# Optimization experiments

Hardware: AMD Instinct MI355X
Metric: run time of the kernel (lower is better)

The kernel has to match this reference:

```python
import jax, jax.numpy as jnp
import numpy as np

D_MODEL = 1024
NUM_HEADS = 16
D_HEAD = D_MODEL // NUM_HEADS
BATCH = 4
SEQ = 2048
NEG_INF = -1e30


def setup_inputs() -> dict:
    key = jax.random.key(0)
    k_x, k_q, k_k, k_v, k_o = jax.random.split(key, 5)
    scale = 1.0 / np.sqrt(D_MODEL)
    x = jax.random.normal(k_x, (BATCH, SEQ, D_MODEL), dtype=jnp.float32)
    Qw = jax.random.normal(k_q, (D_MODEL, D_MODEL), dtype=jnp.float32) * scale
    Kw = jax.random.normal(k_k, (D_MODEL, D_MODEL), dtype=jnp.float32) * scale
    Vw = jax.random.normal(k_v, (D_MODEL, D_MODEL), dtype=jnp.float32) * scale
    Ow = jax.random.normal(k_o, (D_MODEL, D_MODEL), dtype=jnp.float32) * scale
    padding_mask = jnp.zeros((BATCH, SEQ), dtype=bool)  # True = masked position
    return {"x": x, "Qw": Qw, "Kw": Kw, "Vw": Vw, "Ow": Ow, "padding_mask": padding_mask}


def reference(x, Qw, Kw, Vw, Ow, padding_mask):
    B, S, D = x.shape
    H, dh = NUM_HEADS, D_HEAD
    # torch Linear (no bias): y = x @ W.T
    q = jnp.einsum("bsd,ed->bse", x, Qw).reshape(B, S, H, dh)
    k = jnp.einsum("bsd,ed->bse", x, Kw).reshape(B, S, H, dh)
    v = jnp.einsum("bsd,ed->bse", x, Vw).reshape(B, S, H, dh)
    # scores: [B, H, Sq, Sk]
    score = jnp.einsum("bqhd,bkhd->bhqk", q, k) / jnp.sqrt(jnp.float32(dh))
    # causal mask (masked=True)
    causal = jnp.tril(jnp.ones((S, S), dtype=bool))  # True = keep
    score = jnp.where(causal[None, None, :, :], score, NEG_INF)
    # padding mask: True = masked key position
    score = jnp.where(padding_mask[:, None, None, :], NEG_INF, score)
    attn = jax.nn.softmax(score, axis=-1)  # dropout=0.0 (eval mode)
    ctx = jnp.einsum("bhqk,bkhd->bqhd", attn, v).reshape(B, S, D)
    out = jnp.einsum("bsd,ed->bse", ctx, Ow)
    return out
```

## Files before the change

### kernel.cpp

```cpp
#include <hip/hip_runtime.h>
#include <hip/hip_bf16.h>

typedef __attribute__((ext_vector_type(8))) short short8;
typedef __attribute__((ext_vector_type(4))) float f32x4;

#define MFMA_BF16_16x16x32(a,b,c) __builtin_amdgcn_mfma_f32_16x16x32_bf16((a),(b),(c),0,0,0)

constexpr int B_  = 4;
constexpr int S_  = 2048;
constexpr int H_  = 16;
constexpr int DH_ = 64;
constexpr int D_  = 1024;
constexpr int M_  = B_ * S_;

__device__ __forceinline__ unsigned short f2bf(float f) {
  union { float f; unsigned u; } v; v.f = f;
  unsigned u = v.u;
  u += 0x7fffu + ((u >> 16) & 1u);
  return (unsigned short)(u >> 16);
}

__device__ __forceinline__ short8 cvt8(f32x4 a, f32x4 b) {
  union { __hip_bfloat162 h[4]; short8 s; } u;
  u.h[0] = __float22bfloat162_rn(make_float2(a[0], a[1]));
  u.h[1] = __float22bfloat162_rn(make_float2(a[2], a[3]));
  u.h[2] = __float22bfloat162_rn(make_float2(b[0], b[1]));
  u.h[3] = __float22bfloat162_rn(make_float2(b[2], b[3]));
  return u.s;
}

__device__ __forceinline__ unsigned pk2(float a, float b) {
  union { __hip_bfloat162 h; unsigned u; } z;
  z.h = __float22bfloat162_rn(make_float2(a, b));
  return z.u;
}

__global__ __launch_bounds__(256)
void cvt_pre(const float* __restrict__ x, unsigned short* __restrict__ xb,
             const float* __restrict__ Kw, const float* __restrict__ Vw,
             unsigned short* __restrict__ Kwb, unsigned short* __restrict__ Vwb) {
  const int bb = blockIdx.x;
  const float* s;
  unsigned short* d;
  size_t i;
  if (bb < 4096)      { s = x;  d = xb;  i = ((size_t)bb * 256 + threadIdx.x) * 8; }
  else if (bb < 4608) { s = Kw; d = Kwb; i = ((size_t)(bb - 4096) * 256 + threadIdx.x) * 8; }
  else                { s = Vw; d = Vwb; i = ((size_t)(bb - 4608) * 256 + threadIdx.x) * 8; }
  *(short8*)(d + i) = cvt8(*(const f32x4*)(s + i), *(const f32x4*)(s + i + 4));
}

__global__ __launch_bounds__(256)
void cvt_w(const float* __restrict__ s0, unsigned short* __restrict__ d0) {
  const size_t i = ((size_t)blockIdx.x * 256 + threadIdx.x) * 8;
  *(short8*)(d0 + i) = cvt8(*(const f32x4*)(s0 + i), *(const f32x4*)(s0 + i + 4));
}

__device__ __forceinline__ void stage16(const unsigned short* __restrict__ g,
                                        short* lds_wave_base, int lane) {
#if __has_builtin(__builtin_amdgcn_global_load_lds)
  __builtin_amdgcn_global_load_lds(
      (const __attribute__((address_space(1))) unsigned int*)g,
      (__attribute__((address_space(3))) unsigned int*)lds_wave_base, 16, 0, 0);
#else
  *(short8*)(lds_wave_base + lane * 8) = *(const short8*)g;
#endif
}

__global__ __launch_bounds__(256)
void gemm_bb(const unsigned short* __restrict__ xb,
             const unsigned short* __restrict__ Qwb,
             const unsigned short* __restrict__ Kwb,
             const unsigned short* __restrict__ Vwb,
             unsigned short* __restrict__ Qo, unsigned short* __restrict__ Ko,
             unsigned short* __restrict__ VTo, int haveQ) {
  __shared__ __align__(16) short As[128 * 32];
  __shared__ __align__(16) short Bs[128 * 32];

  const int nb  = blockIdx.x;
  const int sel = haveQ ? (nb >> 3) : 1 + (nb >> 3);
  const int n0  = (nb & 7) * 128;
  const unsigned short* Wb = (sel == 0) ? Qwb : (sel == 1) ? Kwb : Vwb;
  unsigned short* out      = (sel == 0) ? Qo  : (sel == 1) ? Ko  : VTo;
  const float scale = (sel == 0) ? 0.125f : 1.0f;
  const int epi = (sel == 2) ? 2 : 1;

  const int tid  = threadIdx.x;
  const int lane = tid & 63;
  const int w    = tid >> 6;
  const int quad = lane >> 4;
  const int l16  = lane & 15;
  const int wm   = (w >> 1) * 64;
  const int wn   = (w & 1) * 64;
  const int m0   = blockIdx.y * 128;

  const int srow = tid >> 2;
  const int scol = (tid & 3) * 8;

  f32x4 acc[4][4];
  #pragma unroll
  for (int i = 0; i < 4; ++i)
    #pragma unroll
    for (int j = 0; j < 4; ++j)
      acc[i][j] = (f32x4){0.f, 0.f, 0.f, 0.f};

  for (int k0 = 0; k0 < D_; k0 += 32) {
    __syncthreads();
    #pragma unroll
    for (int j = 0; j < 2; ++j) {
      const int row = j * 64 + srow;
      stage16(xb + (size_t)(m0 + row) * D_ + k0 + scol, As + j * 2048 + w * 512, lane);
      stage16(Wb + (size_t)(n0 + row) * D_ + k0 + scol, Bs + j * 2048 + w * 512, lane);
    }
    __syncthreads();

    short8 af[4], bf[4];
    #pragma unroll
    for (int i = 0; i < 4; ++i)
      af[i] = *(const short8*)(&As[(wm + i * 16 + l16) * 32 + quad * 8]);
    #pragma unroll
    for (int j = 0; j < 4; ++j)
      bf[j] = *(const short8*)(&Bs[(wn + j * 16 + l16) * 32 + quad * 8]);
    #pragma unroll
    for (int i = 0; i < 4; ++i)
      #pragma unroll
      for (int j = 0; j < 4; ++j)
        acc[i][j] = MFMA_BF16_16x16x32(af[i], bf[j], acc[i][j]);
  }

  #pragma unroll
  for (int i = 0; i < 4; ++i)
    #pragma unroll
    for (int j = 0; j < 4; ++j)
      #pragma unroll
      for (int r = 0; r < 4; ++r) {
        int m = m0 + wm + i * 16 + quad * 4 + r;
        int n = n0 + wn + j * 16 + l16;
        unsigned short bv = f2bf(acc[i][j][r] * scale);
        int b = m >> 11, s = m & (S_ - 1);
        int h = n >> 6,  d = n & (DH_ - 1);
        if (epi == 1)
          out[((size_t)(b * H_ + h) * S_ + s) * DH_ + d] = bv;
        else
          out[((size_t)(b * H_ + h) * DH_ + d) * S_ + s] = bv;
      }
}

__global__ __launch_bounds__(256)
void gemm_out_bb(const unsigned short* __restrict__ A,
                 const unsigned short* __restrict__ Wb,
                 float* __restrict__ out) {
  __shared__ __align__(16) short As[128 * 32];
  __shared__ __align__(16) short Bs[128 * 32];

  const int tid  = threadIdx.x;
  const int lane = tid & 63;
  const int w    = tid >> 6;
  const int quad = lane >> 4;
  const int l16  = lane & 15;
  const int wm   = (w >> 1) * 64;
  const int wn   = (w & 1) * 64;
  const int m0   = blockIdx.y * 128;
  const int n0   = blockIdx.x * 128;

  const int srow = tid >> 2;
  const int scol = (tid & 3) * 8;

  f32x4 acc[4][4];
  #pragma unroll
  for (int i = 0; i < 4; ++i)
    #pragma unroll
    for (int j = 0; j < 4; ++j)
      acc[i][j] = (f32x4){0.f, 0.f, 0.f, 0.f};

  for (int k0 = 0; k0 < D_; k0 += 32) {
    __syncthreads();
    #pragma unroll
    for (int j = 0; j < 2; ++j) {
      const int row = j * 64 + srow;
      stage16(A  + (size_t)(m0 + row) * D_ + k0 + scol, As + j * 2048 + w * 512, lane);
      stage16(Wb + (size_t)(n0 + row) * D_ + k0 + scol, Bs + j * 2048 + w * 512, lane);
    }
    __syncthreads();

    short8 af[4], bf[4];
    #pragma unroll
    for (int i = 0; i < 4; ++i)
      af[i] = *(const short8*)(&As[(wm + i * 16 + l16) * 32 + quad * 8]);
    #pragma unroll
    for (int j = 0; j < 4; ++j)
      bf[j] = *(const short8*)(&Bs[(wn + j * 16 + l16) * 32 + quad * 8]);
    #pragma unroll
    for (int i = 0; i < 4; ++i)
      #pragma unroll
      for (int j = 0; j < 4; ++j)
        acc[i][j] = MFMA_BF16_16x16x32(af[i], bf[j], acc[i][j]);
  }

  #pragma unroll
  for (int i = 0; i < 4; ++i)
    #pragma unroll
    for (int j = 0; j < 4; ++j)
      #pragma unroll
      for (int r = 0; r < 4; ++r) {
        int m = m0 + wm + i * 16 + quad * 4 + r;
        int n = n0 + wn + j * 16 + l16;
        out[(size_t)m * D_ + n] = acc[i][j][r];
      }
}

__global__ __launch_bounds__(256)
void gemm_q_f32w(const unsigned short* __restrict__ xb,
                 const float* __restrict__ Qw,
                 unsigned short* __restrict__ Qo) {
  constexpr int LDK = 40;
  __shared__ __align__(16) short As[128 * LDK];
  __shared__ __align__(16) short Bs[128 * LDK];

  const int tid  = threadIdx.x;
  const int lane = tid & 63;
  const int w    = tid >> 6;
  const int quad = lane >> 4;
  const int l16  = lane & 15;
  const int wm   = (w >> 1) * 64;
  const int wn   = (w & 1) * 64;
  const int m0   = blockIdx.y * 128;
  const int n0   = blockIdx.x * 128;

  f32x4 acc[4][4];
  #pragma unroll
  for (int i = 0; i < 4; ++i)
    #pragma unroll
    for (int j = 0; j < 4; ++j)
      acc[i][j] = (f32x4){0.f, 0.f, 0.f, 0.f};

  for (int k0 = 0; k0 < D_; k0 += 32) {
    __syncthreads();
    #pragma unroll
    for (int i = 0; i < 2; ++i) {
      int flat = i * 256 + tid;
      int row  = flat >> 2;
      int col  = (flat & 3) * 8;
      *(short8*)(&As[row * LDK + col]) =
          *(const short8*)(xb + (size_t)(m0 + row) * D_ + k0 + col);
      const float* Wp = Qw + (size_t)(n0 + row) * D_ + k0 + col;
      *(short8*)(&Bs[row * LDK + col]) = cvt8(*(const f32x4*)Wp, *(const f32x4*)(Wp + 4));
    }
    __syncthreads();

    short8 af[4], bf[4];
    #pragma unroll
    for (int i = 0; i < 4; ++i)
      af[i] = *(const short8*)(&As[(wm + i * 16 + l16) * LDK + quad * 8]);
    #pragma unroll
    for (int j = 0; j < 4; ++j)
      bf[j] = *(const short8*)(&Bs[(wn + j * 16 + l16) * LDK + quad * 8]);
    #pragma unroll
    for (int i = 0; i < 4; ++i)
      #pragma unroll
      for (int j = 0; j < 4; ++j)
        acc[i][j] = MFMA_BF16_16x16x32(af[i], bf[j], acc[i][j]);
  }

  #pragma unroll
  for (int i = 0; i < 4; ++i)
    #pragma unroll
    for (int j = 0; j < 4; ++j)
      #pragma unroll
      for (int r = 0; r < 4; ++r) {
        int m = m0 + wm + i * 16 + quad * 4 + r;
        int n = n0 + wn + j * 16 + l16;
        unsigned short bv = f2bf(acc[i][j][r] * 0.125f);
        int b = m >> 11, s = m & (S_ - 1);
        int h = n >> 6,  d = n & (DH_ - 1);
        Qo[((size_t)(b * H_ + h) * S_ + s) * DH_ + d] = bv;
      }
}

constexpr int LDP_ = 64;

__device__ __forceinline__ void attn_range(
    const unsigned short* __restrict__ Kh,
    const unsigned short* __restrict__ Vh,
    const unsigned char* __restrict__ pmb,
    short* __restrict__ Pw,
    const short8 qf[2][2], f32x4 acc[2][4], f32x4 lacc[2],
    int qw, int kt0, int kt1, int quad, int l16) {
  const short8 ones = {0x3F80, 0x3F80, 0x3F80, 0x3F80,
                       0x3F80, 0x3F80, 0x3F80, 0x3F80};
  if (kt0 >= kt1) return;
  const int key = (l16 & 7) << 4;

  short8 kb[8];
  {
    const int k0 = kt0 * 64;
    #pragma unroll
    for (int t = 0; t < 4; ++t) {
      const unsigned short* kp = Kh + (size_t)(k0 + t * 16 + l16) * DH_ + quad * 8;
      kb[t * 2]     = *(const short8*)(kp);
      kb[t * 2 + 1] = *(const short8*)(kp + 32);
    }
  }

  for (int kt = kt0; kt < kt1; ++kt) {
    const int k0 = kt * 64;

    unsigned pm4[4];
    #pragma unroll
    for (int t = 0; t < 4; ++t)
      pm4[t] = *(const unsigned*)(pmb + k0 + t * 16 + quad * 4);

    f32x4 sc[2][4];
    __builtin_amdgcn_s_setprio(1);
    #pragma unroll
    for (int t = 0; t < 4; ++t) {
      #pragma unroll
      for (int i = 0; i < 2; ++i) {
        f32x4 z = (f32x4){0.f, 0.f, 0.f, 0.f};
        z = MFMA_BF16_16x16x32(kb[t * 2], qf[i][0], z);
        sc[i][t] = MFMA_BF16_16x16x32(kb[t * 2 + 1], qf[i][1], z);
      }
    }
    __builtin_amdgcn_s_setprio(0);

    short8 vb[8];
    #pragma unroll
    for (int t = 0; t < 4; ++t)
      vb[t] = *(const short8*)(Vh + (size_t)(t * 16 + l16) * S_ + k0 + quad * 8);

    #pragma unroll
    for (int i = 0; i < 2; ++i)
      #pragma unroll
      for (int t = 0; t < 4; ++t)
        #pragma unroll
        for (int r = 0; r < 4; ++r) {
          float e = __expf(sc[i][t][r]);
          sc[i][t][r] = ((pm4[t] >> (8 * r)) & 0xffu) ? 0.f : e;
        }
    if (k0 + 63 > qw) {
      #pragma unroll
      for (int t = 0; t < 4; ++t)
        #pragma unroll
        for (int r = 0; r < 4; ++r) {
          int kk = k0 + t * 16 + quad * 4 + r;
          #pragma unroll
          for (int i = 0; i < 2; ++i) {
            int qrow = qw + i * 16 + l16;
            if (kk > qrow) sc[i][t][r] = 0.f;
          }
        }
    }

    #pragma unroll
    for (int i = 0; i < 2; ++i)
      #pragma unroll
      for (int t = 0; t < 4; ++t) {
        unsigned lo = pk2(sc[i][t][0], sc[i][t][1]);
        unsigned hi = pk2(sc[i][t][2], sc[i][t][3]);
        int boff = (i * 16 + l16) * 128 + ((t * 32 + quad * 8) ^ key);
        *(uint2*)((char*)Pw + boff) = make_uint2(lo, hi);
      }

    asm volatile("" ::: "memory");
    {
      const int kn = (kt + 1 < kt1) ? (kt + 1) * 64 : k0;
      #pragma unroll
      for (int t = 0; t < 4; ++t) {
        const unsigned short* kp = Kh + (size_t)(kn + t * 16 + l16) * DH_ + quad * 8;
        kb[t * 2]     = *(const short8*)(kp);
        kb[t * 2 + 1] = *(const short8*)(kp + 32);
      }
    }

    #pragma unroll
    for (int t = 0; t < 4; ++t)
      vb[4 + t] = *(const short8*)(Vh + (size_t)(t * 16 + l16) * S_ + k0 + 32 + quad * 8);

    __builtin_amdgcn_s_setprio(1);
    #pragma unroll
    for (int ks = 0; ks < 2; ++ks) {
      short8 pa0 = *(const short8*)((const char*)Pw +
                    (l16 * 128 + ((ks * 64 + quad * 16) ^ key)));
      short8 pa1 = *(const short8*)((const char*)Pw +
                    ((16 + l16) * 128 + ((ks * 64 + quad * 16) ^ key)));
      #pragma unroll
      for (int t = 0; t < 4; ++t) {
        acc[0][t] = MFMA_BF16_16x16x32(pa0, vb[ks * 4 + t], acc[0][t]);
        acc[1][t] = MFMA_BF16_16x16x32(pa1, vb[ks * 4 + t], acc[1][t]);
      }
      lacc[0] = MFMA_BF16_16x16x32(pa0, ones, lacc[0]);
      lacc[1] = MFMA_BF16_16x16x32(pa1, ones, lacc[1]);
    }
    __builtin_amdgcn_s_setprio(0);
  }
}

__global__ __launch_bounds__(128)
void attn(const unsigned short* __restrict__ Q,
          const unsigned short* __restrict__ K,
          const unsigned short* __restrict__ VT,
          const unsigned char* __restrict__ pmask,
          unsigned short* __restrict__ CTX) {
  __shared__ __align__(16) short Ps[2 * 32 * LDP_];
  __shared__ float Rbuf[64 * 40];

  const int tid  = threadIdx.x;
  const int lane = tid & 63;
  const int w    = tid >> 6;
  const int quad = lane >> 4;
  const int l16  = lane & 15;

  const int L    = blockIdx.x;
  const int xcd  = L & 7;
  const int slot = L >> 3;
  const int bh   = xcd + 8 * (slot & 7);
  const int p    = slot >> 3;
  const int b    = bh >> 4;
  const int h    = bh & 15;

  const int qtA = p, qtB = 63 - p;
  const int ntA = (qtA >> 1) + 1;
  const int ntB = (qtB >> 1) + 1;
  const int splitB = 17 - ntA;

  const unsigned short* Qh = Q  + ((size_t)b * H_ + h) * S_ * DH_;
  const unsigned short* Kh = K  + ((size_t)b * H_ + h) * S_ * DH_;
  const unsigned short* Vh = VT + ((size_t)b * H_ + h) * DH_ * S_;
  const unsigned char* pmb = pmask + (size_t)b * S_;
  unsigned short* CTXb = CTX + (size_t)b * S_ * D_;
  short* Pw = &Ps[w * 32 * LDP_];

  f32x4 acc[2][4];
  f32x4 lacc[2];
  short8 qf[2][2];

  if (w == 0) {
    {
      const int qw = qtA * 32;
      #pragma unroll
      for (int i = 0; i < 2; ++i)
        #pragma unroll
        for (int c = 0; c < 2; ++c)
          qf[i][c] = *(const short8*)(Qh + (size_t)(qw + i * 16 + l16) * DH_ + c * 32 + quad * 8);
      #pragma unroll
      for (int i = 0; i < 2; ++i) {
        #pragma unroll
        for (int t = 0; t < 4; ++t) acc[i][t] = (f32x4){0.f, 0.f, 0.f, 0.f};
        lacc[i] = (f32x4){0.f, 0.f, 0.f, 0.f};
      }
      attn_range(Kh, Vh, pmb, Pw, qf, acc, lacc, qw, 0, ntA, quad, l16);
      #pragma unroll
      for (int i = 0; i < 2; ++i)
        #pragma unroll
        for (int r = 0; r < 4; ++r) {
          int qrow = qw + i * 16 + quad * 4 + r;
          float inv = 1.0f / lacc[i][r];
          #pragma unroll
          for (int t = 0; t < 4; ++t)
            CTXb[(size_t)qrow * D_ + h * DH_ + t * 16 + l16] = f2bf(acc[i][t][r] * inv);
        }
    }
    {
      const int qw = qtB * 32;
      #pragma unroll
      for (int i = 0; i < 2; ++i)
        #pragma unroll
        for (int c = 0; c < 2; ++c)
          qf[i][c] = *(const short8*)(Qh + (size_t)(qw + i * 16 + l16) * DH_ + c * 32 + quad * 8);
      #pragma unroll
      for (int i = 0; i < 2; ++i) {
        #pragma unroll
        for (int t = 0; t < 4; ++t) acc[i][t] = (f32x4){0.f, 0.f, 0.f, 0.f};
        lacc[i] = (f32x4){0.f, 0.f, 0.f, 0.f};
      }
      attn_range(Kh, Vh, pmb, Pw, qf, acc, lacc, qw, 0, splitB, quad, l16);
      __syncthreads();
      #pragma unroll
      for (int i = 0; i < 2; ++i) {
        #pragma unroll
        for (int t = 0; t < 4; ++t)
          #pragma unroll
          for (int r = 0; r < 4; ++r)
            acc[i][t][r] += Rbuf[lane * 40 + i * 16 + t * 4 + r];
        #pragma unroll
        for (int r = 0; r < 4; ++r)
          lacc[i][r] += Rbuf[lane * 40 + 32 + i * 4 + r];
      }
      #pragma unroll
      for (int i = 0; i < 2; ++i)
        #pragma unroll
        for (int r = 0; r < 4; ++r) {
          int qrow = qw + i * 16 + quad * 4 + r;
          float inv = 1.0f / lacc[i][r];
          #pragma unroll
          for (int t = 0; t < 4; ++t)
            CTXb[(size_t)qrow * D_ + h * DH_ + t * 16 + l16] = f2bf(acc[i][t][r] * inv);
        }
    }
  } else {
    const int qw = qtB * 32;
    #pragma unroll
    for (int i = 0; i < 2; ++i)
      #pragma unroll
      for (int c = 0; c < 2; ++c)
        qf[i][c] = *(const short8*)(Qh + (size_t)(qw + i * 16 + l16) * DH_ + c * 32 + quad * 8);
    #pragma unroll
    for (int i = 0; i < 2; ++i) {
      #pragma unroll
      for (int t = 0; t < 4; ++t) acc[i][t] = (f32x4){0.f, 0.f, 0.f, 0.f};
      lacc[i] = (f32x4){0.f, 0.f, 0.f, 0.f};
    }
    attn_range(Kh, Vh, pmb, Pw, qf, acc, lacc, qw, splitB, ntB, quad, l16);
    #pragma unroll
    for (int i = 0; i < 2; ++i) {
      #pragma unroll
      for (int t = 0; t < 4; ++t)
        #pragma unroll
        for (int r = 0; r < 4; ++r)
          Rbuf[lane * 40 + i * 16 + t * 4 + r] = acc[i][t][r];
      #pragma unroll
      for (int r = 0; r < 4; ++r)
        Rbuf[lane * 40 + 32 + i * 4 + r] = lacc[i][r];
    }
    __syncthreads();
  }
}

extern "C" void kernel_launch(void* const* d_in, const int* in_sizes, int n_in,
                              void* d_out, int out_size, void* d_ws, size_t ws_size,
                              hipStream_t stream) {
  const float* x  = (const float*)d_in[0];
  const float* Qw = (const float*)d_in[1];
  const float* Kw = (const float*)d_in[2];
  const float* Vw = (const float*)d_in[3];
  const float* Ow = (const float*)d_in[4];
  const unsigned char* pm = (const unsigned char*)d_in[5];

  const size_t NE = (size_t)M_ * D_;
  const size_t DD = (size_t)D_ * D_;
  unsigned short* Qall  = (unsigned short*)d_out;
  unsigned short* CTXa  = (unsigned short*)d_out + NE;
  unsigned short* ws16  = (unsigned short*)d_ws;
  unsigned short* Kall  = ws16;
  unsigned short* VTall = ws16 + NE;
  unsigned short* Owb   = VTall;

  unsigned short* Kwb = Qall;
  unsigned short* Vwb = Qall + DD;

  cvt_pre<<<dim3(4096 + 1024), 256, 0, stream>>>(x, CTXa, Kw, Vw, Kwb, Vwb);

  gemm_bb<<<dim3(16, M_ / 128), 256, 0, stream>>>(CTXa, nullptr, Kwb, Vwb,
                                                  Qall, Kall, VTall, 0);
  gemm_q_f32w<<<dim3(8, M_ / 128), 256, 0, stream>>>(CTXa, Qw, Qall);

  attn<<<dim3(2048), 128, 0, stream>>>(Qall, Kall, VTall, pm, CTXa);

  cvt_w<<<dim3(512), 256, 0, stream>>>(Ow, Owb);

  hipMemcpyAsync(d_ws, (const void*)CTXa, NE * sizeof(unsigned short),
                 hipMemcpyDeviceToDevice, stream);

  gemm_out_bb<<<dim3(D_ / 128, M_ / 128), 256, 0, stream>>>(ws16, Owb,
                                                            (float*)d_out);
}
```

Measured before the change: 378.6 us.

## Fuse Q projection into bf16 QKV gemm, drop K prefetch, pad Rbuf

When the workspace is large enough, all four weight matrices are converted to bf16 in one combined kernel. The Q projection then joins the K/V bf16 gemm in a single 24-column launch, replacing the separate fp32-weight Q gemm and the later Ow conversion kernel. The attention inner loop drops the software prefetch of the next K tile and loads K at the top of each iteration, which cuts register pressure but exposes load latency. The reduction buffer stride is padded from 40 to 41 floats to avoid LDS bank conflicts.

```diff
diff --git a/kernel.cpp b/kernel.cpp
--- a/kernel.cpp
+++ b/kernel.cpp
@@ -36,16 +36,23 @@
 }
 
 __global__ __launch_bounds__(256)
-void cvt_pre(const float* __restrict__ x, unsigned short* __restrict__ xb,
-             const float* __restrict__ Kw, const float* __restrict__ Vw,
-             unsigned short* __restrict__ Kwb, unsigned short* __restrict__ Vwb) {
+void cvt_many(const float* __restrict__ x,  unsigned short* __restrict__ xb,
+              const float* __restrict__ s1, unsigned short* __restrict__ d1,
+              const float* __restrict__ s2, unsigned short* __restrict__ d2,
+              const float* __restrict__ s3, unsigned short* __restrict__ d3,
+              const float* __restrict__ s4, unsigned short* __restrict__ d4) {
   const int bb = blockIdx.x;
   const float* s;
   unsigned short* d;
   size_t i;
-  if (bb < 4096)      { s = x;  d = xb;  i = ((size_t)bb * 256 + threadIdx.x) * 8; }
-  else if (bb < 4608) { s = Kw; d = Kwb; i = ((size_t)(bb - 4096) * 256 + threadIdx.x) * 8; }
-  else                { s = Vw; d = Vwb; i = ((size_t)(bb - 4608) * 256 + threadIdx.x) * 8; }
+  if (bb < 4096) { s = x; d = xb; i = ((size_t)bb * 256 + threadIdx.x) * 8; }
+  else {
+    const int a = (bb - 4096) >> 9;
+    const int r = (bb - 4096) & 511;
+    s = (a == 0) ? s1 : (a == 1) ? s2 : (a == 2) ? s3 : s4;
+    d = (a == 0) ? d1 : (a == 1) ? d2 : (a == 2) ? d3 : d4;
+    i = ((size_t)r * 256 + threadIdx.x) * 8;
+  }
   *(short8*)(d + i) = cvt8(*(const f32x4*)(s + i), *(const f32x4*)(s + i + 4));
 }
 
@@ -287,23 +294,18 @@
     int qw, int kt0, int kt1, int quad, int l16) {
   const short8 ones = {0x3F80, 0x3F80, 0x3F80, 0x3F80,
                        0x3F80, 0x3F80, 0x3F80, 0x3F80};
-  if (kt0 >= kt1) return;
   const int key = (l16 & 7) << 4;
 
-  short8 kb[8];
-  {
-    const int k0 = kt0 * 64;
+  for (int kt = kt0; kt < kt1; ++kt) {
+    const int k0 = kt * 64;
+
+    short8 kb[8];
     #pragma unroll
     for (int t = 0; t < 4; ++t) {
       const unsigned short* kp = Kh + (size_t)(k0 + t * 16 + l16) * DH_ + quad * 8;
       kb[t * 2]     = *(const short8*)(kp);
       kb[t * 2 + 1] = *(const short8*)(kp + 32);
     }
-  }
-
-  for (int kt = kt0; kt < kt1; ++kt) {
-    const int k0 = kt * 64;
-
     unsigned pm4[4];
     #pragma unroll
     for (int t = 0; t < 4; ++t)
@@ -360,17 +362,6 @@
         *(uint2*)((char*)Pw + boff) = make_uint2(lo, hi);
       }
 
-    asm volatile("" ::: "memory");
-    {
-      const int kn = (kt + 1 < kt1) ? (kt + 1) * 64 : k0;
-      #pragma unroll
-      for (int t = 0; t < 4; ++t) {
-        const unsigned short* kp = Kh + (size_t)(kn + t * 16 + l16) * DH_ + quad * 8;
-        kb[t * 2]     = *(const short8*)(kp);
-        kb[t * 2 + 1] = *(const short8*)(kp + 32);
-      }
-    }
-
     #pragma unroll
     for (int t = 0; t < 4; ++t)
       vb[4 + t] = *(const short8*)(Vh + (size_t)(t * 16 + l16) * S_ + k0 + 32 + quad * 8);
@@ -401,7 +392,7 @@
           const unsigned char* __restrict__ pmask,
           unsigned short* __restrict__ CTX) {
   __shared__ __align__(16) short Ps[2 * 32 * LDP_];
-  __shared__ float Rbuf[64 * 40];
+  __shared__ float Rbuf[64 * 41];
 
   const int tid  = threadIdx.x;
   const int lane = tid & 63;
@@ -480,10 +471,10 @@
         for (int t = 0; t < 4; ++t)
           #pragma unroll
           for (int r = 0; r < 4; ++r)
-            acc[i][t][r] += Rbuf[lane * 40 + i * 16 + t * 4 + r];
+            acc[i][t][r] += Rbuf[lane * 41 + i * 16 + t * 4 + r];
         #pragma unroll
         for (int r = 0; r < 4; ++r)
-          lacc[i][r] += Rbuf[lane * 40 + 32 + i * 4 + r];
+          lacc[i][r] += Rbuf[lane * 41 + 32 + i * 4 + r];
       }
       #pragma unroll
       for (int i = 0; i < 2; ++i)
@@ -516,10 +507,10 @@
       for (int t = 0; t < 4; ++t)
         #pragma unroll
         for (int r = 0; r < 4; ++r)
-          Rbuf[lane * 40 + i * 16 + t * 4 + r] = acc[i][t][r];
+          Rbuf[lane * 41 + i * 16 + t * 4 + r] = acc[i][t][r];
       #pragma unroll
       for (int r = 0; r < 4; ++r)
-        Rbuf[lane * 40 + 32 + i * 4 + r] = lacc[i][r];
+        Rbuf[lane * 41 + 32 + i * 4 + r] = lacc[i][r];
     }
     __syncthreads();
   }
@@ -542,24 +533,48 @@
   unsigned short* ws16  = (unsigned short*)d_ws;
   unsigned short* Kall  = ws16;
   unsigned short* VTall = ws16 + NE;
-  unsigned short* Owb   = VTall;
-
-  unsigned short* Kwb = Qall;
-  unsigned short* Vwb = Qall + DD;
-
-  cvt_pre<<<dim3(4096 + 1024), 256, 0, stream>>>(x, CTXa, Kw, Vw, Kwb, Vwb);
-
-  gemm_bb<<<dim3(16, M_ / 128), 256, 0, stream>>>(CTXa, nullptr, Kwb, Vwb,
-                                                  Qall, Kall, VTall, 0);
-  gemm_q_f32w<<<dim3(8, M_ / 128), 256, 0, stream>>>(CTXa, Qw, Qall);
-
-  attn<<<dim3(2048), 128, 0, stream>>>(Qall, Kall, VTall, pm, CTXa);
-
-  cvt_w<<<dim3(512), 256, 0, stream>>>(Ow, Owb);
-
-  hipMemcpyAsync(d_ws, (const void*)CTXa, NE * sizeof(unsigned short),
-                 hipMemcpyDeviceToDevice, stream);
-
-  gemm_out_bb<<<dim3(D_ / 128, M_ / 128), 256, 0, stream>>>(ws16, Owb,
-                                                            (float*)d_out);
-}
+
+  const bool tail = ws_size >= (2 * NE + 4 * DD) * sizeof(unsigned short);
+
+  if (tail) {
+    unsigned short* Qwb = ws16 + 2 * NE;
+    unsigned short* Kwb = Qwb + DD;
+    unsigned short* Vwb = Kwb + DD;
+    unsigned short* Owb = Vwb + DD;
+
+    cvt_many<<<dim3(4096 + 4 * 512), 256, 0, stream>>>(
+        x, CTXa, Qw, Qwb, Kw, Kwb, Vw, Vwb, Ow, Owb);
+
+    gemm_bb<<<dim3(24, M_ / 128), 256, 0, stream>>>(CTXa, Qwb, Kwb, Vwb,
+                                                    Qall, Kall, VTall, 1);
+
+    attn<<<dim3(2048), 128, 0, stream>>>(Qall, Kall, VTall, pm, CTXa);
+
+    hipMemcpyAsync(d_ws, (const void*)CTXa, NE * sizeof(unsigned short),
+                   hipMemcpyDeviceToDevice, stream);
+
+    gemm_out_bb<<<dim3(D_ / 128, M_ / 128), 256, 0, stream>>>(ws16, Owb,
+                                                              (float*)d_out);
+  } else {
+    unsigned short* Kwb = Qall;
+    unsigned short* Vwb = Qall + DD;
+    unsigned short* Owb = VTall;
+
+    cvt_many<<<dim3(4096 + 2 * 512), 256, 0, stream>>>(
+        x, CTXa, Kw, Kwb, Vw, Vwb, Vw, Vwb, Vw, Vwb);
+
+    gemm_bb<<<dim3(16, M_ / 128), 256, 0, stream>>>(CTXa, nullptr, Kwb, Vwb,
+                                                    Qall, Kall, VTall, 0);
+    gemm_q_f32w<<<dim3(8, M_ / 128), 256, 0, stream>>>(CTXa, Qw, Qall);
+
+    attn<<<dim3(2048), 128, 0, stream>>>(Qall, Kall, VTall, pm, CTXa);
+
+    cvt_w<<<dim3(512), 256, 0, stream>>>(Ow, Owb);
+
+    hipMemcpyAsync(d_ws, (const void*)CTXa, NE * sizeof(unsigned short),
+                   hipMemcpyDeviceToDevice, stream);
+
+    gemm_out_bb<<<dim3(D_ / 128, M_ / 128), 256, 0, stream>>>(ws16, Owb,
+                                                              (float*)d_out);
+  }
+}
```

Result: faster. 343.7 us (-9.2%).
